# Kernel optimization log

Measured on AMD Instinct MI355X. Metric: run time of the kernel, lower is better.

Reference implementation:

```python
import jax, jax.numpy as jnp
import numpy as np

N, E, G = 100000, 1600000, 128
IN, HID, HEADS, EDIM, OUT = 16, 32, 4, 8, 4
HC = HEADS * HID


def _p(k, shape):
    return jax.random.normal(k, shape, jnp.float32) * 0.1


def setup_inputs():
    key = jax.random.key(0)
    ks = list(jax.random.split(key, 24))
    nxt = iter(ks)
    d = dict(
        x=jax.random.normal(next(nxt), (N, IN), jnp.float32),
        edge_index=jax.random.randint(next(nxt), (2, E), 0, N),
        edge_attr=jax.random.normal(next(nxt), (E, EDIM), jnp.float32),
        batch=jnp.sort(jax.random.randint(next(nxt), (N,), 0, G)),
    )
    # conv1: in=IN -> heads*hid
    d['wl1'] = _p(next(nxt), (IN, HC));  d['bl1'] = jnp.zeros((HC,), jnp.float32)
    d['wr1'] = _p(next(nxt), (IN, HC));  d['br1'] = jnp.zeros((HC,), jnp.float32)
    d['we1'] = _p(next(nxt), (EDIM, HC)); d['att1'] = _p(next(nxt), (HEADS, HID)); d['bc1'] = jnp.zeros((HC,), jnp.float32)
    # conv2: in=HC -> heads*hid
    d['wl2'] = _p(next(nxt), (HC, HC));  d['bl2'] = jnp.zeros((HC,), jnp.float32)
    d['wr2'] = _p(next(nxt), (HC, HC));  d['br2'] = jnp.zeros((HC,), jnp.float32)
    d['we2'] = _p(next(nxt), (EDIM, HC)); d['att2'] = _p(next(nxt), (HEADS, HID)); d['bc2'] = jnp.zeros((HC,), jnp.float32)
    # conv3: in=HC -> 1*hid (heads=1)
    d['wl3'] = _p(next(nxt), (HC, HID)); d['bl3'] = jnp.zeros((HID,), jnp.float32)
    d['wr3'] = _p(next(nxt), (HC, HID)); d['br3'] = jnp.zeros((HID,), jnp.float32)
    d['we3'] = _p(next(nxt), (EDIM, HID)); d['att3'] = _p(next(nxt), (1, HID)); d['bc3'] = jnp.zeros((HID,), jnp.float32)
    d['w_fc1'] = _p(next(nxt), (HID, 2 * HID)); d['b_fc1'] = jnp.zeros((2 * HID,), jnp.float32)
    d['w_fc2'] = _p(next(nxt), (2 * HID, OUT)); d['b_fc2'] = jnp.zeros((OUT,), jnp.float32)
    return d


def _gatv2(x, src, dst, eattr, wl, bl, wr, br, we, att, bias, n):
    # PyG GATv2Conv: e_ij = a^T . leaky_relu(Wl x_j + Wr x_i + We e_ij)
    H, C = att.shape
    xl = (x @ wl + bl).reshape(-1, H, C)  # source transform [N,H,C]
    xr = (x @ wr + br).reshape(-1, H, C)  # target transform [N,H,C]
    ea = (eattr @ we).reshape(-1, H, C)   # edge transform   [E,H,C]
    e = jax.nn.leaky_relu(xl[src] + xr[dst] + ea, 0.2)  # [E,H,C]
    logit = jnp.einsum('ehc,hc->eh', e, att)            # [E,H]
    m = jax.ops.segment_max(logit, dst, num_segments=n)
    p = jnp.exp(logit - m[dst])
    s = jax.ops.segment_sum(p, dst, num_segments=n)
    alpha = p / (s[dst] + 1e-16)                        # segment softmax per dst
    out = jax.ops.segment_sum(xl[src] * alpha[:, :, None], dst, num_segments=n)
    return out.reshape(n, H * C) + bias


def reference(x, edge_index, edge_attr, batch,
              wl1, bl1, wr1, br1, we1, att1, bc1,
              wl2, bl2, wr2, br2, we2, att2, bc2,
              wl3, bl3, wr3, br3, we3, att3, bc3,
              w_fc1, b_fc1, w_fc2, b_fc2):
    n = x.shape[0]
    src, dst = edge_index[0], edge_index[1]
    # add_self_loops=True with fill_value='mean' (mean of incoming edge_attr per node)
    ones_e = jnp.ones((src.shape[0],), x.dtype)
    cnt = jax.ops.segment_sum(ones_e, dst, num_segments=n)
    loop_attr = jax.ops.segment_sum(edge_attr, dst, num_segments=n) / jnp.maximum(cnt, 1.0)[:, None]
    ar = jnp.arange(n)
    src_a = jnp.concatenate([src, ar])
    dst_a = jnp.concatenate([dst, ar])
    ea = jnp.concatenate([edge_attr, loop_attr], axis=0)

    h = jax.nn.elu(_gatv2(x, src_a, dst_a, ea, wl1, bl1, wr1, br1, we1, att1, bc1, n))
    h = jax.nn.elu(_gatv2(h, src_a, dst_a, ea, wl2, bl2, wr2, br2, we2, att2, bc2, n))
    h = jax.nn.elu(_gatv2(h, src_a, dst_a, ea, wl3, bl3, wr3, br3, we3, att3, bc3, n))

    # global mean pool over graphs
    gs = jax.ops.segment_sum(h, batch, num_segments=G)
    gc = jax.ops.segment_sum(jnp.ones((n,), h.dtype), batch, num_segments=G)
    g = gs / jnp.maximum(gc, 1.0)[:, None]

    g = jax.nn.elu(g @ w_fc1 + b_fc1)
    return g @ w_fc2 + b_fc2
```

## Files before the change

### kernel.cpp

```cpp
#include <hip/hip_runtime.h>
#include <cstdint>
#include <type_traits>

constexpr int GNUM = 128;

typedef _Float16 h2 __attribute__((ext_vector_type(2)));
typedef _Float16 h4 __attribute__((ext_vector_type(4)));
typedef _Float16 h8 __attribute__((ext_vector_type(8)));
typedef float f4 __attribute__((ext_vector_type(4)));


__global__ __launch_bounds__(256) void hist_kernel(const int* __restrict__ dst,
                                                   int* __restrict__ cnt, int E) {
  int i = blockIdx.x * 256 + threadIdx.x;
  if (i < E) atomicAdd(&cnt[dst[i]], 1);
}

__global__ __launch_bounds__(256) void scan_part_kernel(const int* __restrict__ cnt,
                                                        int* __restrict__ bpart, int n) {
  __shared__ int red[256];
  int base = blockIdx.x * 512;
  int t = threadIdx.x;
  int s = 0;
  int i0 = base + t, i1 = base + 256 + t;
  if (i0 < n) s += cnt[i0] + 1;
  if (i1 < n) s += cnt[i1] + 1;
  red[t] = s;
  __syncthreads();
  for (int off = 128; off > 0; off >>= 1) {
    if (t < off) red[t] += red[t + off];
    __syncthreads();
  }
  if (t == 0) bpart[blockIdx.x] = red[0];
}

__global__ __launch_bounds__(1024) void scan_top_kernel(const int* __restrict__ bpart,
                                                        int* __restrict__ boff,
                                                        int* __restrict__ row_ptr,
                                                        const int* __restrict__ batch,
                                                        int* __restrict__ gstart,
                                                        int B, int n) {
  __shared__ int buf[1024];
  int t = threadIdx.x;
  buf[t] = (t < B) ? bpart[t] : 0;
  __syncthreads();
  for (int off = 1; off < 1024; off <<= 1) {
    int v = (t >= off) ? buf[t - off] : 0;
    __syncthreads();
    buf[t] += v;
    __syncthreads();
  }
  if (t < B) boff[t] = (t == 0) ? 0 : buf[t - 1];
  if (t == 0) row_ptr[n] = buf[1023];
  if (t <= GNUM) {
    int lo = 0, hi = n;
    while (lo < hi) {
      int mid = (lo + hi) >> 1;
      if (batch[mid] < t) lo = mid + 1; else hi = mid;
    }
    gstart[t] = lo;
  }
}

__global__ __launch_bounds__(256) void scan_write_kernel(const int* __restrict__ cnt,
                                                         const int* __restrict__ boff,
                                                         int* __restrict__ row_ptr,
                                                         int* __restrict__ fill, int n) {
  __shared__ int red[256];
  int base = blockIdx.x * 512;
  int t = threadIdx.x;
  int i0 = base + 2 * t, i1 = base + 2 * t + 1;
  int v0 = (i0 < n) ? cnt[i0] + 1 : 0;
  int v1 = (i1 < n) ? cnt[i1] + 1 : 0;
  int val = v0 + v1;
  red[t] = val;
  __syncthreads();
  for (int off = 1; off < 256; off <<= 1) {
    int u = (t >= off) ? red[t - off] : 0;
    __syncthreads();
    red[t] += u;
    __syncthreads();
  }
  int o = boff[blockIdx.x] + red[t] - val;
  if (i0 < n) { row_ptr[i0] = o; fill[i0] = o; }
  if (i1 < n) { row_ptr[i1] = o + v0; fill[i1] = o + v0; }
}

__global__ __launch_bounds__(256) void scatter_kernel(const int* __restrict__ src,
                                                      const int* __restrict__ dst,
                                                      const float* __restrict__ ea,
                                                      int* __restrict__ fill,
                                                      int* __restrict__ csr_src,
                                                      _Float16* __restrict__ ea_csr, int E) {
  int i = blockIdx.x * 256 + threadIdx.x;
  if (i >= E) return;
  int d = dst[i];
  int p = atomicAdd(&fill[d], 1);
  csr_src[p] = src[i];
  float4 e0 = *(const float4*)&ea[(size_t)i * 8];
  float4 e1 = *(const float4*)&ea[(size_t)i * 8 + 4];
  h8 v;
  v[0] = (_Float16)e0.x; v[1] = (_Float16)e0.y; v[2] = (_Float16)e0.z; v[3] = (_Float16)e0.w;
  v[4] = (_Float16)e1.x; v[5] = (_Float16)e1.y; v[6] = (_Float16)e1.z; v[7] = (_Float16)e1.w;
  *(h8*)&ea_csr[(size_t)p * 8] = v;
}

__global__ __launch_bounds__(256) void selfloop_kernel(const int* __restrict__ row_ptr,
                                                       int* __restrict__ csr_src,
                                                       _Float16* __restrict__ ea_csr, int n) {
  int idx = blockIdx.x * 256 + threadIdx.x;
  int i = idx >> 3, c = idx & 7;
  if (i >= n) return;
  int s = row_ptr[i], e = row_ptr[i + 1] - 1;
  float a = 0.f;
  for (int j = s; j < e; j++) a += (float)ea_csr[(size_t)j * 8 + c];
  float inv = 1.f / fmaxf((float)(e - s), 1.f);
  ea_csr[(size_t)e * 8 + c] = (_Float16)(a * inv);
  if (c == 0) csr_src[e] = i;
}

__global__ __launch_bounds__(256) void pack_all_kernel(
    const float* __restrict__ wl1, _Float16* __restrict__ p1l,
    const float* __restrict__ wr1, _Float16* __restrict__ p1r,
    const float* __restrict__ wl2, _Float16* __restrict__ p2l,
    const float* __restrict__ wr2, _Float16* __restrict__ p2r,
    const float* __restrict__ wl3, _Float16* __restrict__ p3l,
    const float* __restrict__ wr3, _Float16* __restrict__ p3r) {
  int y = blockIdx.y;
  const float* w; _Float16* wp; int Kreal, Kpad, NC;
  switch (y) {
    case 0: w = wl1; wp = p1l; Kreal = 16;  Kpad = 32;  NC = 128; break;
    case 1: w = wr1; wp = p1r; Kreal = 16;  Kpad = 32;  NC = 128; break;
    case 2: w = wl2; wp = p2l; Kreal = 128; Kpad = 128; NC = 128; break;
    case 3: w = wr2; wp = p2r; Kreal = 128; Kpad = 128; NC = 128; break;
    case 4: w = wl3; wp = p3l; Kreal = 128; Kpad = 128; NC = 32;  break;
    default: w = wr3; wp = p3r; Kreal = 128; Kpad = 128; NC = 32; break;
  }
  int KB = Kpad / 32;
  int total = (NC / 16) * KB * 64;
  int idx = blockIdx.x * 256 + threadIdx.x;
  if (idx >= total) return;
  int lane = idx & 63;
  int blk = idx >> 6;
  int nt = blk / KB, kb = blk % KB;
  int col = nt * 16 + (lane & 15);
  int krow = kb * 32 + (lane >> 4) * 8;
  h8 v;
#pragma unroll
  for (int j = 0; j < 8; j++)
    v[j] = (krow + j < Kreal) ? (_Float16)w[(size_t)(krow + j) * NC + col] : (_Float16)0.f;
  *(h8*)&wp[(size_t)idx * 8] = v;
}


template <int K, int NCOLS>
__global__ __launch_bounds__(256) void k1m_kernel(const _Float16* __restrict__ x,
                                                  const _Float16* __restrict__ wp0,
                                                  const float* __restrict__ b0,
                                                  _Float16* __restrict__ out0,
                                                  const _Float16* __restrict__ wp1,
                                                  const float* __restrict__ b1,
                                                  _Float16* __restrict__ out1, int n) {
  constexpr int NT = NCOLS / 16, KB = K / 32;
  const _Float16* wp = blockIdx.y ? wp1 : wp0;
  const float* b = blockIdx.y ? b1 : b0;
  _Float16* out = blockIdx.y ? out1 : out0;

  int tid = threadIdx.x;
  int wave = tid >> 6, lane = tid & 63;
  int m = lane & 15, quad = lane >> 4;
  int node0 = blockIdx.x * 64 + wave * 16;

  h8 afrag[KB];
  int anode = node0 + m;
  if (anode < n) {
#pragma unroll
    for (int kb = 0; kb < KB; kb++)
      afrag[kb] = *(const h8*)&x[(size_t)anode * K + kb * 32 + quad * 8];
  } else {
#pragma unroll
    for (int kb = 0; kb < KB; kb++) afrag[kb] = (h8)(_Float16)0.f;
  }

  f4 acc[NT] = {};
#pragma unroll
  for (int nt = 0; nt < NT; nt++) {
#pragma unroll
    for (int kb = 0; kb < KB; kb++) {
      h8 bfrag = *(const h8*)&wp[((size_t)(nt * KB + kb) * 64 + lane) * 8];
      acc[nt] = __builtin_amdgcn_mfma_f32_16x16x32_f16(afrag[kb], bfrag, acc[nt], 0, 0, 0);
    }
  }

#pragma unroll
  for (int nt = 0; nt < NT; nt++) {
#pragma unroll
    for (int r = 0; r < 4; r++) {
      int row = node0 + quad * 4 + r;
      if (row < n) {
        int col = nt * 16 + m;
        out[(size_t)row * NCOLS + col] = (_Float16)(acc[nt][r] + b[col]);
      }
    }
  }
}

template <int NCOLS>
__global__ __launch_bounds__(256) void k1m16_kernel(const float* __restrict__ x,
                                                    const _Float16* __restrict__ wp0,
                                                    const float* __restrict__ b0,
                                                    _Float16* __restrict__ out0,
                                                    const _Float16* __restrict__ wp1,
                                                    const float* __restrict__ b1,
                                                    _Float16* __restrict__ out1, int n) {
  constexpr int NT = NCOLS / 16;
  const _Float16* wp = blockIdx.y ? wp1 : wp0;
  const float* b = blockIdx.y ? b1 : b0;
  _Float16* out = blockIdx.y ? out1 : out0;

  int tid = threadIdx.x;
  int wave = tid >> 6, lane = tid & 63;
  int m = lane & 15, quad = lane >> 4;
  int node0 = blockIdx.x * 64 + wave * 16;

  int anode = node0 + m;
  h8 afrag = (h8)(_Float16)0.f;
  if (anode < n && quad < 2) {
    float4 v0 = *(const float4*)&x[(size_t)anode * 16 + quad * 8];
    float4 v1 = *(const float4*)&x[(size_t)anode * 16 + quad * 8 + 4];
    afrag[0] = (_Float16)v0.x; afrag[1] = (_Float16)v0.y;
    afrag[2] = (_Float16)v0.z; afrag[3] = (_Float16)v0.w;
    afrag[4] = (_Float16)v1.x; afrag[5] = (_Float16)v1.y;
    afrag[6] = (_Float16)v1.z; afrag[7] = (_Float16)v1.w;
  }

  f4 acc[NT] = {};
#pragma unroll
  for (int nt = 0; nt < NT; nt++) {
    h8 bfrag = *(const h8*)&wp[((size_t)nt * 64 + lane) * 8];
    acc[nt] = __builtin_amdgcn_mfma_f32_16x16x32_f16(afrag, bfrag, acc[nt], 0, 0, 0);
  }

#pragma unroll
  for (int nt = 0; nt < NT; nt++) {
#pragma unroll
    for (int r = 0; r < 4; r++) {
      int row = node0 + quad * 4 + r;
      if (row < n) {
        int col = nt * 16 + m;
        out[(size_t)row * NCOLS + col] = (_Float16)(acc[nt][r] + b[col]);
      }
    }
  }
}

__global__ __launch_bounds__(256) void k2w_kernel(
    const _Float16* __restrict__ xl, const _Float16* __restrict__ xr,
    const int* __restrict__ row_ptr, const int* __restrict__ csr_src,
    const _Float16* __restrict__ ea_csr, const float* __restrict__ we,
    const float* __restrict__ att, const float* __restrict__ bc,
    _Float16* __restrict__ out, int n) {
  int tid = threadIdx.x;
  int lane = tid & 63;
  int node = blockIdx.x * 4 + (tid >> 6);
  if (node >= n) return;
  int c0 = lane << 1;

  h2 w2[8];
#pragma unroll
  for (int k = 0; k < 8; k++) {
    float2 v = *(const float2*)&we[k * 128 + c0];
    w2[k] = h2{(_Float16)v.x, (_Float16)v.y};
  }
  const float LOG2E = 1.44269504088896f;
  float2 av = *(const float2*)&att[c0];
  h2 a2 = h2{(_Float16)(av.x * LOG2E), (_Float16)(av.y * LOG2E)};
  h2 xr2 = *(const h2*)&xr[(size_t)node * 128 + c0];
  const h2 p2 = h2{(_Float16)0.2f, (_Float16)0.2f};

  int start = __builtin_amdgcn_readfirstlane(row_ptr[node]);
  int end   = __builtin_amdgcn_readfirstlane(row_ptr[node + 1]);

  float s = 0.f, acc0 = 0.f, acc1 = 0.f;
  int j = start;

  if ((end - start) & 1) {
    int s0 = __builtin_amdgcn_readfirstlane(csr_src[j]);
    h8 e0 = *(const h8*)&ea_csr[(size_t)j * 8];
    h2 x0 = *(const h2*)&xl[(uint32_t)s0 * 128u + (uint32_t)c0];
    h2 t0 = x0 + xr2;
#pragma unroll
    for (int k = 0; k < 8; k++) t0 += h2{e0[k], e0[k]} * w2[k];
    t0 = __builtin_elementwise_max(t0, t0 * p2);
    h2 pd0 = t0 * a2;
    float part0 = (float)pd0[0] + (float)pd0[1];
    part0 += __shfl_xor(part0, 1, 64);
    part0 += __shfl_xor(part0, 2, 64);
    part0 += __shfl_xor(part0, 4, 64);
    part0 += __shfl_xor(part0, 8, 64);
    float pe0 = __builtin_amdgcn_exp2f(part0);
    s += pe0;
    acc0 += pe0 * (float)x0[0];
    acc1 += pe0 * (float)x0[1];
    j++;
  }

  if (j < end) {
    int base = j;
    int pairs = (end - j) >> 1;
    int s0 = __builtin_amdgcn_readfirstlane(csr_src[j]);
    int s1 = __builtin_amdgcn_readfirstlane(csr_src[j + 1]);
    h8 e0 = *(const h8*)&ea_csr[(size_t)j * 8];
    h8 e1 = *(const h8*)&ea_csr[((size_t)j + 1) * 8];
    h2 x0 = *(const h2*)&xl[(uint32_t)s0 * 128u + (uint32_t)c0];
    h2 x1 = *(const h2*)&xl[(uint32_t)s1 * 128u + (uint32_t)c0];

#pragma unroll 2
    for (int p = 0; p < pairs; p++) {
      int jn = j + 2 * (p + 1);
      int kp = (jn < end) ? jn : base;
      int ns0 = __builtin_amdgcn_readfirstlane(csr_src[kp]);
      int ns1 = __builtin_amdgcn_readfirstlane(csr_src[kp + 1]);
      h8 ne0 = *(const h8*)&ea_csr[(size_t)kp * 8];
      h8 ne1 = *(const h8*)&ea_csr[((size_t)kp + 1) * 8];

      h2 t0 = x0 + xr2;
      h2 t1 = x1 + xr2;
#pragma unroll
      for (int k = 0; k < 8; k++) {
        t0 += h2{e0[k], e0[k]} * w2[k];
        t1 += h2{e1[k], e1[k]} * w2[k];
      }
      t0 = __builtin_elementwise_max(t0, t0 * p2);
      t1 = __builtin_elementwise_max(t1, t1 * p2);
      h2 pd0 = t0 * a2;
      h2 pd1 = t1 * a2;
      float part0 = (float)pd0[0] + (float)pd0[1];
      float part1 = (float)pd1[0] + (float)pd1[1];

      h2 nx0 = *(const h2*)&xl[(uint32_t)ns0 * 128u + (uint32_t)c0];
      h2 nx1 = *(const h2*)&xl[(uint32_t)ns1 * 128u + (uint32_t)c0];

      part0 += __shfl_xor(part0, 1, 64);
      part1 += __shfl_xor(part1, 1, 64);
      part0 += __shfl_xor(part0, 2, 64);
      part1 += __shfl_xor(part1, 2, 64);
      part0 += __shfl_xor(part0, 4, 64);
      part1 += __shfl_xor(part1, 4, 64);
      part0 += __shfl_xor(part0, 8, 64);
      part1 += __shfl_xor(part1, 8, 64);
      float pe0 = __builtin_amdgcn_exp2f(part0);
      float pe1 = __builtin_amdgcn_exp2f(part1);
      s += pe0 + pe1;
      acc0 += pe0 * (float)x0[0] + pe1 * (float)x1[0];
      acc1 += pe0 * (float)x0[1] + pe1 * (float)x1[1];

      e0 = ne0; e1 = ne1; x0 = nx0; x1 = nx1;
    }
  }

  float inv = 1.f / (s + 1e-16f);
  float2 bv = *(const float2*)&bc[c0];
  float v0 = acc0 * inv + bv.x;
  float v1 = acc1 * inv + bv.y;
  v0 = v0 > 0.f ? v0 : (__expf(v0) - 1.f);
  v1 = v1 > 0.f ? v1 : (__expf(v1) - 1.f);
  *(h2*)&out[(size_t)node * 128 + c0] = h2{(_Float16)v0, (_Float16)v1};
}

template <int H>
__global__ __launch_bounds__(128) void k2_kernel(
    const _Float16* __restrict__ xl, const _Float16* __restrict__ xr,
    const int* __restrict__ row_ptr, const int* __restrict__ csr_src,
    const _Float16* __restrict__ ea_csr, const float* __restrict__ we,
    const float* __restrict__ att, const float* __restrict__ bc,
    _Float16* __restrict__ out, int n) {
  constexpr int HC = H * 32;
  constexpr int NL = HC / 4;
  constexpr int NPB = 128 / NL;

  int tid = threadIdx.x;
  int ln = tid / NL, q = tid % NL;
  int c0 = 4 * q;
  int node = blockIdx.x * NPB + ln;
  if (node >= n) return;

  h2 w2[8][2];
#pragma unroll
  for (int k = 0; k < 8; k++) {
    float4 v = *(const float4*)&we[k * HC + c0];
    w2[k][0] = h2{(_Float16)v.x, (_Float16)v.y};
    w2[k][1] = h2{(_Float16)v.z, (_Float16)v.w};
  }
  const float LOG2E = 1.44269504088896f;
  float4 av = *(const float4*)&att[c0];
  h2 a0 = h2{(_Float16)(av.x * LOG2E), (_Float16)(av.y * LOG2E)};
  h2 a1 = h2{(_Float16)(av.z * LOG2E), (_Float16)(av.w * LOG2E)};
  h4 xrh = *(const h4*)&xr[(size_t)node * HC + c0];
  h2 xr0 = h2{xrh[0], xrh[1]}, xr1 = h2{xrh[2], xrh[3]};
  const h2 p2 = h2{(_Float16)0.2f, (_Float16)0.2f};

  float acc[4] = {0.f, 0.f, 0.f, 0.f};
  float s = 0.f;

  int start = row_ptr[node], end = row_ptr[node + 1];
  int len = end - start;
  int pairs = (len + 1) >> 1;

  int j1 = (start + 1 < end) ? start + 1 : start;
  float m1 = (start + 1 < end) ? 1.f : 0.f;
  int s0 = csr_src[start], s1 = csr_src[j1];
  h8 e0 = *(const h8*)&ea_csr[(size_t)start * 8];
  h8 e1 = *(const h8*)&ea_csr[(size_t)j1 * 8];
  h4 x0 = *(const h4*)&xl[(size_t)s0 * HC + c0];
  h4 x1 = *(const h4*)&xl[(size_t)s1 * HC + c0];

#pragma unroll 2
  for (int p = 0; p < pairs; p++) {
    int jn = start + 2 * (p + 1);
    int k0 = (jn < end) ? jn : start;
    int k1 = (jn + 1 < end) ? jn + 1 : k0;
    float nm1 = (jn + 1 < end) ? 1.f : 0.f;
    int ns0 = csr_src[k0], ns1 = csr_src[k1];
    h8 ne0 = *(const h8*)&ea_csr[(size_t)k0 * 8];
    h8 ne1 = *(const h8*)&ea_csr[(size_t)k1 * 8];

    h2 t00 = h2{x0[0], x0[1]} + xr0;
    h2 t01 = h2{x0[2], x0[3]} + xr1;
    h2 t10 = h2{x1[0], x1[1]} + xr0;
    h2 t11 = h2{x1[2], x1[3]} + xr1;
#pragma unroll
    for (int k = 0; k < 8; k++) {
      h2 ev0 = h2{e0[k], e0[k]};
      h2 ev1 = h2{e1[k], e1[k]};
      t00 += ev0 * w2[k][0];
      t01 += ev0 * w2[k][1];
      t10 += ev1 * w2[k][0];
      t11 += ev1 * w2[k][1];
    }
    t00 = __builtin_elementwise_max(t00, t00 * p2);
    t01 = __builtin_elementwise_max(t01, t01 * p2);
    t10 = __builtin_elementwise_max(t10, t10 * p2);
    t11 = __builtin_elementwise_max(t11, t11 * p2);
    h2 pd0 = t00 * a0 + t01 * a1;
    h2 pd1 = t10 * a0 + t11 * a1;
    float part0 = (float)pd0[0] + (float)pd0[1];
    float part1 = (float)pd1[0] + (float)pd1[1];

    h4 nx0 = *(const h4*)&xl[(size_t)ns0 * HC + c0];
    h4 nx1 = *(const h4*)&xl[(size_t)ns1 * HC + c0];

    part0 += __shfl_xor(part0, 1, 64);
    part1 += __shfl_xor(part1, 1, 64);
    part0 += __shfl_xor(part0, 2, 64);
    part1 += __shfl_xor(part1, 2, 64);
    part0 += __shfl_xor(part0, 4, 64);
    part1 += __shfl_xor(part1, 4, 64);
    float pe0 = __builtin_amdgcn_exp2f(part0);
    float pe1 = __builtin_amdgcn_exp2f(part1) * m1;
    s += pe0 + pe1;
#pragma unroll
    for (int i = 0; i < 4; i++)
      acc[i] += pe0 * (float)x0[i] + pe1 * (float)x1[i];

    s0 = ns0; s1 = ns1; e0 = ne0; e1 = ne1; x0 = nx0; x1 = nx1; m1 = nm1;
  }

  float inv = 1.f / (s + 1e-16f);
  h4 o;
#pragma unroll
  for (int i = 0; i < 4; i++) {
    float v = acc[i] * inv + bc[c0 + i];
    o[i] = (_Float16)(v > 0.f ? v : (__expf(v) - 1.f));
  }
  *(h4*)&out[(size_t)node * HC + c0] = o;
}

__global__ __launch_bounds__(256) void poolfc_kernel(const _Float16* __restrict__ h,
                                                     const int* __restrict__ gstart,
                                                     const float* __restrict__ w1,
                                                     const float* __restrict__ b1,
                                                     const float* __restrict__ w2,
                                                     const float* __restrict__ b2,
                                                     float* __restrict__ out) {
  __shared__ float red[256];
  __shared__ float g[32];
  __shared__ float a1[64];
  int gi = blockIdx.x;
  int t = threadIdx.x;
  int s = gstart[gi], e = gstart[gi + 1];
  int c = t & 31, rg = t >> 5;
  float acc = 0.f;
  for (int i = s + rg; i < e; i += 8) acc += (float)h[(size_t)i * 32 + c];
  red[t] = acc;
  __syncthreads();
  if (t < 128) red[t] += red[t + 128];
  __syncthreads();
  if (t < 64) red[t] += red[t + 64];
  __syncthreads();
  if (t < 32) g[t] = (red[t] + red[t + 32]) / fmaxf((float)(e - s), 1.f);
  __syncthreads();
  if (t < 64) {
    float v = b1[t];
    for (int k = 0; k < 32; k++) v += g[k] * w1[k * 64 + t];
    a1[t] = v > 0.f ? v : (__expf(v) - 1.f);
  }
  __syncthreads();
  if (t < 4) {
    float o = b2[t];
    for (int k = 0; k < 64; k++) o += a1[k] * w2[k * 4 + t];
    out[gi * 4 + t] = o;
  }
}


extern "C" void kernel_launch(void* const* d_in, const int* in_sizes, int n_in,
                              void* d_out, int out_size, void* d_ws, size_t ws_size,
                              hipStream_t stream) {
  const float* x     = (const float*)d_in[0];
  const int*   ei    = (const int*)d_in[1];
  const float* eattr = (const float*)d_in[2];
  const int*   batch = (const int*)d_in[3];
  const float *wl1 = (const float*)d_in[4],  *bl1 = (const float*)d_in[5];
  const float *wr1 = (const float*)d_in[6],  *br1 = (const float*)d_in[7];
  const float *we1 = (const float*)d_in[8],  *at1 = (const float*)d_in[9];
  const float *bc1 = (const float*)d_in[10];
  const float *wl2 = (const float*)d_in[11], *bl2 = (const float*)d_in[12];
  const float *wr2 = (const float*)d_in[13], *br2 = (const float*)d_in[14];
  const float *we2 = (const float*)d_in[15], *at2 = (const float*)d_in[16];
  const float *bc2 = (const float*)d_in[17];
  const float *wl3 = (const float*)d_in[18], *bl3 = (const float*)d_in[19];
  const float *wr3 = (const float*)d_in[20], *br3 = (const float*)d_in[21];
  const float *we3 = (const float*)d_in[22], *at3 = (const float*)d_in[23];
  const float *bc3 = (const float*)d_in[24];
  const float *wf1 = (const float*)d_in[25], *bf1 = (const float*)d_in[26];
  const float *wf2 = (const float*)d_in[27], *bf2 = (const float*)d_in[28];

  int N = in_sizes[0] / 16;
  int E = in_sizes[1] / 2;
  const int* srcp = ei;
  const int* dstp = ei + E;
  int EA = E + N;
  int NB = (N + 511) / 512;

  char* wsb = (char*)d_ws;
  size_t off = 0;
  auto alloc = [&](size_t bytes) -> char* {
    char* p = wsb + off;
    off += (bytes + 255) & ~(size_t)255;
    return p;
  };
  int*       cnt     = (int*)alloc((size_t)N * 4);
  int*       row_ptr = (int*)alloc((size_t)(N + 1) * 4);
  int*       fill    = (int*)alloc((size_t)N * 4);
  int*       bpart   = (int*)alloc((size_t)1024 * 4);
  int*       boff    = (int*)alloc((size_t)1024 * 4);
  int*       csr_src = (int*)alloc((size_t)EA * 4);
  _Float16*  ea_csr  = (_Float16*)alloc((size_t)EA * 8 * 2);
  _Float16*  xl      = (_Float16*)alloc((size_t)N * 128 * 2);
  _Float16*  xr      = (_Float16*)alloc((size_t)N * 128 * 2);
  _Float16*  h16     = (_Float16*)alloc((size_t)N * 128 * 2);
  _Float16*  h3      = (_Float16*)alloc((size_t)N * 32 * 2);
  int*       gstart  = (int*)alloc((size_t)(GNUM + 1) * 4);
  _Float16*  wp1l    = (_Float16*)alloc((size_t)32 * 128 * 2);
  _Float16*  wp1r    = (_Float16*)alloc((size_t)32 * 128 * 2);
  _Float16*  wp2l    = (_Float16*)alloc((size_t)128 * 128 * 2);
  _Float16*  wp2r    = (_Float16*)alloc((size_t)128 * 128 * 2);
  _Float16*  wp3l    = (_Float16*)alloc((size_t)128 * 32 * 2);
  _Float16*  wp3r    = (_Float16*)alloc((size_t)128 * 32 * 2);

  hipMemsetAsync(cnt, 0, (size_t)N * 4, stream);

  hist_kernel<<<(E + 255) / 256, 256, 0, stream>>>(dstp, cnt, E);
  scan_part_kernel<<<NB, 256, 0, stream>>>(cnt, bpart, N);
  scan_top_kernel<<<1, 1024, 0, stream>>>(bpart, boff, row_ptr, batch, gstart, NB, N);
  scan_write_kernel<<<NB, 256, 0, stream>>>(cnt, boff, row_ptr, fill, N);
  scatter_kernel<<<(E + 255) / 256, 256, 0, stream>>>(srcp, dstp, eattr, fill, csr_src, ea_csr, E);
  selfloop_kernel<<<(N * 8 + 255) / 256, 256, 0, stream>>>(row_ptr, csr_src, ea_csr, N);
  pack_all_kernel<<<dim3(8, 6), 256, 0, stream>>>(wl1, wp1l, wr1, wp1r,
                                                  wl2, wp2l, wr2, wp2r,
                                                  wl3, wp3l, wr3, wp3r);

  k1m16_kernel<128><<<dim3((N + 63) / 64, 2), 256, 0, stream>>>(
      x, wp1l, bl1, xl, wp1r, br1, xr, N);
  k2w_kernel<<<(N + 3) / 4, 256, 0, stream>>>(xl, xr, row_ptr, csr_src, ea_csr,
                                              we1, at1, bc1, h16, N);
  k1m_kernel<128, 128><<<dim3((N + 63) / 64, 2), 256, 0, stream>>>(
      h16, wp2l, bl2, xl, wp2r, br2, xr, N);
  k2w_kernel<<<(N + 3) / 4, 256, 0, stream>>>(xl, xr, row_ptr, csr_src, ea_csr,
                                              we2, at2, bc2, h16, N);
  k1m_kernel<128, 32><<<dim3((N + 63) / 64, 2), 256, 0, stream>>>(
      h16, wp3l, bl3, xl, wp3r, br3, xr, N);
  k2_kernel<1><<<(N + 15) / 16, 128, 0, stream>>>(xl, xr, row_ptr, csr_src, ea_csr,
                                                  we3, at3, bc3, h3, N);

  poolfc_kernel<<<GNUM, 256, 0, stream>>>(h3, gstart, wf1, bf1, wf2, bf2, (float*)d_out);
}
```

Measured before the change: 719.8 us.

## Deepen gather prefetch, use DPP reductions and fdot2 in GATv2 aggregation kernels

Result: faster. 679.4 us (-5.6%).

```diff
diff --git a/kernel.cpp b/kernel.cpp
--- a/kernel.cpp
+++ b/kernel.cpp
@@ -8,6 +8,23 @@
 typedef _Float16 h4 __attribute__((ext_vector_type(4)));
 typedef _Float16 h8 __attribute__((ext_vector_type(8)));
 typedef float f4 __attribute__((ext_vector_type(4)));
+
+template <int CTRL>
+__device__ __forceinline__ float dppadd(float v) {
+  union U { float f; int i; };
+  U u, r;
+  u.f = v;
+  r.i = __builtin_amdgcn_update_dpp(0, u.i, CTRL, 0xF, 0xF, true);
+  return v + r.f;
+}
+
+__device__ __forceinline__ float hdot2(h2 a, h2 b, float c) {
+#if __has_builtin(__builtin_amdgcn_fdot2)
+  return __builtin_amdgcn_fdot2(a, b, c, false);
+#else
+  return c + (float)a[0] * (float)b[0] + (float)a[1] * (float)b[1];
+#endif
+}
 
 
 __global__ __launch_bounds__(256) void hist_kernel(const int* __restrict__ dst,
@@ -266,6 +283,18 @@
   if (node >= n) return;
   int c0 = lane << 1;
 
+  int start = __builtin_amdgcn_readfirstlane(row_ptr[node]);
+  int end   = __builtin_amdgcn_readfirstlane(row_ptr[node + 1]);
+  int len = end - start;
+  int pairs = (len + 1) >> 1;
+
+  int j1 = (start + 1 < end) ? start + 1 : start;
+  float m1 = (start + 1 < end) ? 1.f : 0.f;
+  int s0 = __builtin_amdgcn_readfirstlane(csr_src[start]);
+  int s1 = __builtin_amdgcn_readfirstlane(csr_src[j1]);
+  h8 e0 = *(const h8*)&ea_csr[(size_t)start * 8];
+  h8 e1 = *(const h8*)&ea_csr[(size_t)j1 * 8];
+
   h2 w2[8];
 #pragma unroll
   for (int k = 0; k < 8; k++) {
@@ -278,85 +307,57 @@
   h2 xr2 = *(const h2*)&xr[(size_t)node * 128 + c0];
   const h2 p2 = h2{(_Float16)0.2f, (_Float16)0.2f};
 
-  int start = __builtin_amdgcn_readfirstlane(row_ptr[node]);
-  int end   = __builtin_amdgcn_readfirstlane(row_ptr[node + 1]);
+  h2 x0 = *(const h2*)&xl[(uint32_t)s0 * 128u + (uint32_t)c0];
+  h2 x1 = *(const h2*)&xl[(uint32_t)s1 * 128u + (uint32_t)c0];
+
+  int jn = start + 2;
+  int k0 = (jn < end) ? jn : start;
+  int k1 = (jn + 1 < end) ? jn + 1 : k0;
+  float m1n = (jn + 1 < end) ? 1.f : 0.f;
+  int s0n = __builtin_amdgcn_readfirstlane(csr_src[k0]);
+  int s1n = __builtin_amdgcn_readfirstlane(csr_src[k1]);
+  h8 e0n = *(const h8*)&ea_csr[(size_t)k0 * 8];
+  h8 e1n = *(const h8*)&ea_csr[(size_t)k1 * 8];
 
   float s = 0.f, acc0 = 0.f, acc1 = 0.f;
-  int j = start;
-
-  if ((end - start) & 1) {
-    int s0 = __builtin_amdgcn_readfirstlane(csr_src[j]);
-    h8 e0 = *(const h8*)&ea_csr[(size_t)j * 8];
-    h2 x0 = *(const h2*)&xl[(uint32_t)s0 * 128u + (uint32_t)c0];
+
+#pragma unroll 2
+  for (int p = 0; p < pairs; p++) {
+    int ja = start + 2 * (p + 2);
+    int ka0 = (ja < end) ? ja : start;
+    int ka1 = (ja + 1 < end) ? ja + 1 : ka0;
+    float m1a = (ja + 1 < end) ? 1.f : 0.f;
+    int s0a = __builtin_amdgcn_readfirstlane(csr_src[ka0]);
+    int s1a = __builtin_amdgcn_readfirstlane(csr_src[ka1]);
+    h8 e0a = *(const h8*)&ea_csr[(size_t)ka0 * 8];
+    h8 e1a = *(const h8*)&ea_csr[(size_t)ka1 * 8];
+
+    h2 x0n = *(const h2*)&xl[(uint32_t)s0n * 128u + (uint32_t)c0];
+    h2 x1n = *(const h2*)&xl[(uint32_t)s1n * 128u + (uint32_t)c0];
+
     h2 t0 = x0 + xr2;
-#pragma unroll
-    for (int k = 0; k < 8; k++) t0 += h2{e0[k], e0[k]} * w2[k];
+    h2 t1 = x1 + xr2;
+#pragma unroll
+    for (int k = 0; k < 8; k++) {
+      t0 += h2{e0[k], e0[k]} * w2[k];
+      t1 += h2{e1[k], e1[k]} * w2[k];
+    }
     t0 = __builtin_elementwise_max(t0, t0 * p2);
-    h2 pd0 = t0 * a2;
-    float part0 = (float)pd0[0] + (float)pd0[1];
-    part0 += __shfl_xor(part0, 1, 64);
-    part0 += __shfl_xor(part0, 2, 64);
-    part0 += __shfl_xor(part0, 4, 64);
-    part0 += __shfl_xor(part0, 8, 64);
+    t1 = __builtin_elementwise_max(t1, t1 * p2);
+    float part0 = hdot2(t0, a2, 0.f);
+    float part1 = hdot2(t1, a2, 0.f);
+    part0 = dppadd<0xB1>(part0);   part1 = dppadd<0xB1>(part1);
+    part0 = dppadd<0x4E>(part0);   part1 = dppadd<0x4E>(part1);
+    part0 = dppadd<0x141>(part0);  part1 = dppadd<0x141>(part1);
+    part0 = dppadd<0x140>(part0);  part1 = dppadd<0x140>(part1);
     float pe0 = __builtin_amdgcn_exp2f(part0);
-    s += pe0;
-    acc0 += pe0 * (float)x0[0];
-    acc1 += pe0 * (float)x0[1];
-    j++;
-  }
-
-  if (j < end) {
-    int base = j;
-    int pairs = (end - j) >> 1;
-    int s0 = __builtin_amdgcn_readfirstlane(csr_src[j]);
-    int s1 = __builtin_amdgcn_readfirstlane(csr_src[j + 1]);
-    h8 e0 = *(const h8*)&ea_csr[(size_t)j * 8];
-    h8 e1 = *(const h8*)&ea_csr[((size_t)j + 1) * 8];
-    h2 x0 = *(const h2*)&xl[(uint32_t)s0 * 128u + (uint32_t)c0];
-    h2 x1 = *(const h2*)&xl[(uint32_t)s1 * 128u + (uint32_t)c0];
-
-#pragma unroll 2
-    for (int p = 0; p < pairs; p++) {
-      int jn = j + 2 * (p + 1);
-      int kp = (jn < end) ? jn : base;
-      int ns0 = __builtin_amdgcn_readfirstlane(csr_src[kp]);
-      int ns1 = __builtin_amdgcn_readfirstlane(csr_src[kp + 1]);
-      h8 ne0 = *(const h8*)&ea_csr[(size_t)kp * 8];
-      h8 ne1 = *(const h8*)&ea_csr[((size_t)kp + 1) * 8];
-
-      h2 t0 = x0 + xr2;
-      h2 t1 = x1 + xr2;
-#pragma unroll
-      for (int k = 0; k < 8; k++) {
-        t0 += h2{e0[k], e0[k]} * w2[k];
-        t1 += h2{e1[k], e1[k]} * w2[k];
-      }
-      t0 = __builtin_elementwise_max(t0, t0 * p2);
-      t1 = __builtin_elementwise_max(t1, t1 * p2);
-      h2 pd0 = t0 * a2;
-      h2 pd1 = t1 * a2;
-      float part0 = (float)pd0[0] + (float)pd0[1];
-      float part1 = (float)pd1[0] + (float)pd1[1];
-
-      h2 nx0 = *(const h2*)&xl[(uint32_t)ns0 * 128u + (uint32_t)c0];
-      h2 nx1 = *(const h2*)&xl[(uint32_t)ns1 * 128u + (uint32_t)c0];
-
-      part0 += __shfl_xor(part0, 1, 64);
-      part1 += __shfl_xor(part1, 1, 64);
-      part0 += __shfl_xor(part0, 2, 64);
-      part1 += __shfl_xor(part1, 2, 64);
-      part0 += __shfl_xor(part0, 4, 64);
-      part1 += __shfl_xor(part1, 4, 64);
-      part0 += __shfl_xor(part0, 8, 64);
-      part1 += __shfl_xor(part1, 8, 64);
-      float pe0 = __builtin_amdgcn_exp2f(part0);
-      float pe1 = __builtin_amdgcn_exp2f(part1);
-      s += pe0 + pe1;
-      acc0 += pe0 * (float)x0[0] + pe1 * (float)x1[0];
-      acc1 += pe0 * (float)x0[1] + pe1 * (float)x1[1];
-
-      e0 = ne0; e1 = ne1; x0 = nx0; x1 = nx1;
-    }
+    float pe1 = __builtin_amdgcn_exp2f(part1) * m1;
+    s += pe0 + pe1;
+    acc0 += pe0 * (float)x0[0] + pe1 * (float)x1[0];
+    acc1 += pe0 * (float)x0[1] + pe1 * (float)x1[1];
+
+    x0 = x0n; x1 = x1n; e0 = e0n; e1 = e1n; m1 = m1n;
+    s0n = s0a; s1n = s1a; e0n = e0a; e1n = e1a; m1n = m1a;
   }
 
   float inv = 1.f / (s + 1e-16f);
@@ -442,20 +443,15 @@
     t01 = __builtin_elementwise_max(t01, t01 * p2);
     t10 = __builtin_elementwise_max(t10, t10 * p2);
     t11 = __builtin_elementwise_max(t11, t11 * p2);
-    h2 pd0 = t00 * a0 + t01 * a1;
-    h2 pd1 = t10 * a0 + t11 * a1;
-    float part0 = (float)pd0[0] + (float)pd0[1];
-    float part1 = (float)pd1[0] + (float)pd1[1];
+    float part0 = hdot2(t00, a0, hdot2(t01, a1, 0.f));
+    float part1 = hdot2(t10, a0, hdot2(t11, a1, 0.f));
 
     h4 nx0 = *(const h4*)&xl[(size_t)ns0 * HC + c0];
     h4 nx1 = *(const h4*)&xl[(size_t)ns1 * HC + c0];
 
-    part0 += __shfl_xor(part0, 1, 64);
-    part1 += __shfl_xor(part1, 1, 64);
-    part0 += __shfl_xor(part0, 2, 64);
-    part1 += __shfl_xor(part1, 2, 64);
-    part0 += __shfl_xor(part0, 4, 64);
-    part1 += __shfl_xor(part1, 4, 64);
+    part0 = dppadd<0xB1>(part0);   part1 = dppadd<0xB1>(part1);
+    part0 = dppadd<0x4E>(part0);   part1 = dppadd<0x4E>(part1);
+    part0 = dppadd<0x141>(part0);  part1 = dppadd<0x141>(part1);
     float pe0 = __builtin_amdgcn_exp2f(part0);
     float pe1 = __builtin_amdgcn_exp2f(part1) * m1;
     s += pe0 + pe1;
@@ -483,22 +479,32 @@
                                                      const float* __restrict__ w2,
                                                      const float* __restrict__ b2,
                                                      float* __restrict__ out) {
-  __shared__ float red[256];
+  __shared__ float redx[256];
+  __shared__ float redy[256];
   __shared__ float g[32];
   __shared__ float a1[64];
   int gi = blockIdx.x;
   int t = threadIdx.x;
   int s = gstart[gi], e = gstart[gi + 1];
-  int c = t & 31, rg = t >> 5;
-  float acc = 0.f;
-  for (int i = s + rg; i < e; i += 8) acc += (float)h[(size_t)i * 32 + c];
-  red[t] = acc;
-  __syncthreads();
-  if (t < 128) red[t] += red[t + 128];
-  __syncthreads();
-  if (t < 64) red[t] += red[t + 64];
-  __syncthreads();
-  if (t < 32) g[t] = (red[t] + red[t + 32]) / fmaxf((float)(e - s), 1.f);
+  int cp = t & 15, rg = t >> 4;
+  float ax = 0.f, ay = 0.f;
+  for (int i = s + rg; i < e; i += 16) {
+    h2 v = *(const h2*)&h[(size_t)i * 32 + cp * 2];
+    ax += (float)v[0]; ay += (float)v[1];
+  }
+  redx[t] = ax; redy[t] = ay;
+  __syncthreads();
+  if (t < 128) { redx[t] += redx[t + 128]; redy[t] += redy[t + 128]; }
+  __syncthreads();
+  if (t < 64) { redx[t] += redx[t + 64]; redy[t] += redy[t + 64]; }
+  __syncthreads();
+  if (t < 32) { redx[t] += redx[t + 32]; redy[t] += redy[t + 32]; }
+  __syncthreads();
+  if (t < 16) {
+    float inv = 1.f / fmaxf((float)(e - s), 1.f);
+    g[2 * t]     = (redx[t] + redx[t + 16]) * inv;
+    g[2 * t + 1] = (redy[t] + redy[t + 16]) * inv;
+  }
   __syncthreads();
   if (t < 64) {
     float v = b1[t];
```
